# Kernel tuning notes

Hardware: AMD Instinct MI355X
Metric: run time of the kernel (lower is better)

Reference implementation:

```python
import jax, jax.numpy as jnp
import numpy as np

SIZE = 4096       # reservoir width
STEPS = 512       # num_steps
BETA = 1.0        # leak factor (LSMNeuron default beta=1.0)
THRESHOLD = 10.0  # LSMNeuron threshold=10

# Heaviside spike with atan surrogate gradient (snntorch default surrogate)
@jax.custom_vjp
def heaviside(x):
    return (x > 0).astype(x.dtype)

def _h_fwd(x):
    return (x > 0).astype(x.dtype), x

def _h_bwd(x, g):
    # snntorch ATan surrogate with alpha=2: d/dx = 1 / (1 + (pi*x)^2)
    return (g / (1.0 + (jnp.pi * x) ** 2),)

heaviside.defvjp(_h_fwd, _h_bwd)


def setup_inputs() -> dict:
    key = jax.random.key(0)
    kx, kw = jax.random.split(key)
    x = jax.random.normal(kx, (STEPS, SIZE), dtype=jnp.float32)
    # fc1 weight: Linear(2*size, size), no bias. Input half | recurrent half.
    W = jax.random.normal(kw, (SIZE, 2 * SIZE), dtype=jnp.float32) / np.sqrt(2 * SIZE)
    return {"x": x, "W": W}


def reference(x, W):
    # Split weight: Wx acts on the external input, Ws on recurrent spikes.
    Wx = W[:, :SIZE]   # [size, size]
    Ws = W[:, SIZE:]   # [size, size]
    # Precompute the input-driven current for all steps as one big GEMM.
    cur_x = jnp.einsum('ts,os->to', x, Wx)  # [steps, size]

    def step(carry, cur_xt):
        spk, mem = carry
        cur = cur_xt + Ws @ spk            # fc1(concat(x[t], spk))
        mem = BETA * mem + cur             # leaky integrate
        spk = heaviside(mem - THRESHOLD)   # fire
        mem = mem - spk * THRESHOLD        # subtract reset
        return (spk, mem), (spk, mem)

    init = (jnp.zeros((SIZE,), jnp.float32), jnp.zeros((SIZE,), jnp.float32))
    _, (spk_rec, mem_rec) = jax.lax.scan(step, init, cur_x)
    # original detaches spk_rec
    return jax.lax.stop_gradient(spk_rec), mem_rec
```

## Files before the change

### kernel.cpp

```cpp
#include <hip/hip_runtime.h>

#define N_SIZE 4096
#define N_STEPS 512
#define WROW 8192
#define THRESH 10.0f

__global__ __launch_bounds__(256) void k_transpose(const float* __restrict__ W,
                                                   float* __restrict__ WsT) {
    __shared__ float tile[32][33];
    const int bs = blockIdx.x * 32;
    const int bo = blockIdx.y * 32;
    const int tx = threadIdx.x;
    const int ty = threadIdx.y;
#pragma unroll
    for (int j = 0; j < 4; ++j) {
        const int o = bo + ty + j * 8;
        tile[ty + j * 8][tx] = W[(size_t)o * WROW + N_SIZE + bs + tx];
    }
    __syncthreads();
#pragma unroll
    for (int j = 0; j < 4; ++j) {
        const int s = bs + ty + j * 8;
        WsT[(size_t)s * N_SIZE + bo + tx] = tile[tx][ty + j * 8];
    }
}

#define BM 64
#define BN 128
#define BK 16

__global__ __launch_bounds__(256) void k_gemm(const float* __restrict__ x,
                                              const float* __restrict__ W,
                                              float* __restrict__ C) {
    __shared__ float As[BK][BM + 4];
    __shared__ float Bs[BK][BN + 4];
    const int tid = threadIdx.x;
    const int bm = blockIdx.y * BM;
    const int bn = blockIdx.x * BN;
    const int m0 = (tid >> 4) << 2;
    const int n0 = (tid & 15) << 3;
    const int lr = tid >> 2;
    const int lc = (tid & 3) << 2;

    float acc[4][8];
#pragma unroll
    for (int i = 0; i < 4; ++i)
#pragma unroll
        for (int j = 0; j < 8; ++j) acc[i][j] = 0.f;

    for (int kb = 0; kb < N_SIZE; kb += BK) {
        const float4 a  = *(const float4*)&x[(size_t)(bm + lr) * N_SIZE + kb + lc];
        const float4 b0 = *(const float4*)&W[(size_t)(bn + lr) * WROW + kb + lc];
        const float4 b1 = *(const float4*)&W[(size_t)(bn + 64 + lr) * WROW + kb + lc];
        __syncthreads();
        As[lc + 0][lr] = a.x;  As[lc + 1][lr] = a.y;
        As[lc + 2][lr] = a.z;  As[lc + 3][lr] = a.w;
        Bs[lc + 0][lr] = b0.x; Bs[lc + 1][lr] = b0.y;
        Bs[lc + 2][lr] = b0.z; Bs[lc + 3][lr] = b0.w;
        Bs[lc + 0][64 + lr] = b1.x; Bs[lc + 1][64 + lr] = b1.y;
        Bs[lc + 2][64 + lr] = b1.z; Bs[lc + 3][64 + lr] = b1.w;
        __syncthreads();
#pragma unroll
        for (int k = 0; k < BK; ++k) {
            const float4 av  = *(const float4*)&As[k][m0];
            const float4 bv0 = *(const float4*)&Bs[k][n0];
            const float4 bv1 = *(const float4*)&Bs[k][n0 + 4];
            const float am[4]  = {av.x, av.y, av.z, av.w};
            const float bnv[8] = {bv0.x, bv0.y, bv0.z, bv0.w,
                                  bv1.x, bv1.y, bv1.z, bv1.w};
#pragma unroll
            for (int i = 0; i < 4; ++i)
#pragma unroll
                for (int j = 0; j < 8; ++j)
                    acc[i][j] = fmaf(am[i], bnv[j], acc[i][j]);
        }
    }
#pragma unroll
    for (int i = 0; i < 4; ++i) {
        float* cp = &C[(size_t)(bm + m0 + i) * N_SIZE + bn + n0];
        const float4 o0 = {acc[i][0], acc[i][1], acc[i][2], acc[i][3]};
        const float4 o1 = {acc[i][4], acc[i][5], acc[i][6], acc[i][7]};
        *(float4*)&cp[0] = o0;
        *(float4*)&cp[4] = o1;
    }
}

template <int USE_WST>
__global__ __launch_bounds__(1024) void k_scan(const float* __restrict__ WsT,
                                               const float* __restrict__ W,
                                               float* __restrict__ spk_out,
                                               float* __restrict__ mem_out) {
    __shared__ int lists[2][N_SIZE];
    __shared__ int wcnt[16];
    const int tid  = threadIdx.x;
    const int wave = tid >> 6;
    const int lane = tid & 63;
    const int base = tid << 2;

    float4 mem = {0.f, 0.f, 0.f, 0.f};
    int cnt = 0;
    int cur = 0;

    for (int t = 0; t < N_STEPS; ++t) {
        float* mrow = &mem_out[(size_t)t * N_SIZE + base];
        float4 c = *(const float4*)mrow;

        const int* lst = lists[cur];
        int i = 0;
        for (; i + 2 <= cnt; i += 2) {
            const int s0 = lst[i];
            const int s1 = lst[i + 1];
            float4 w0, w1;
            if (USE_WST) {
                w0 = *(const float4*)&WsT[(size_t)s0 * N_SIZE + base];
                w1 = *(const float4*)&WsT[(size_t)s1 * N_SIZE + base];
            } else {
                w0.x = W[(size_t)(base + 0) * WROW + N_SIZE + s0];
                w0.y = W[(size_t)(base + 1) * WROW + N_SIZE + s0];
                w0.z = W[(size_t)(base + 2) * WROW + N_SIZE + s0];
                w0.w = W[(size_t)(base + 3) * WROW + N_SIZE + s0];
                w1.x = W[(size_t)(base + 0) * WROW + N_SIZE + s1];
                w1.y = W[(size_t)(base + 1) * WROW + N_SIZE + s1];
                w1.z = W[(size_t)(base + 2) * WROW + N_SIZE + s1];
                w1.w = W[(size_t)(base + 3) * WROW + N_SIZE + s1];
            }
            c.x += w0.x + w1.x;
            c.y += w0.y + w1.y;
            c.z += w0.z + w1.z;
            c.w += w0.w + w1.w;
        }
        if (i < cnt) {
            const int s0 = lst[i];
            float4 w0;
            if (USE_WST) {
                w0 = *(const float4*)&WsT[(size_t)s0 * N_SIZE + base];
            } else {
                w0.x = W[(size_t)(base + 0) * WROW + N_SIZE + s0];
                w0.y = W[(size_t)(base + 1) * WROW + N_SIZE + s0];
                w0.z = W[(size_t)(base + 2) * WROW + N_SIZE + s0];
                w0.w = W[(size_t)(base + 3) * WROW + N_SIZE + s0];
            }
            c.x += w0.x; c.y += w0.y; c.z += w0.z; c.w += w0.w;
        }

        mem.x += c.x; mem.y += c.y; mem.z += c.z; mem.w += c.w;

        const bool s0 = mem.x > THRESH;
        const bool s1 = mem.y > THRESH;
        const bool s2 = mem.z > THRESH;
        const bool s3 = mem.w > THRESH;
        if (s0) mem.x -= THRESH;
        if (s1) mem.y -= THRESH;
        if (s2) mem.z -= THRESH;
        if (s3) mem.w -= THRESH;

        const float4 spkv = {s0 ? 1.f : 0.f, s1 ? 1.f : 0.f,
                             s2 ? 1.f : 0.f, s3 ? 1.f : 0.f};
        *(float4*)&spk_out[(size_t)t * N_SIZE + base] = spkv;
        *(float4*)mrow = mem;

        const unsigned long long b0 = __ballot(s0);
        const unsigned long long b1 = __ballot(s1);
        const unsigned long long b2 = __ballot(s2);
        const unsigned long long b3 = __ballot(s3);
        const unsigned long long below =
            (lane == 0) ? 0ULL : (~0ULL >> (64 - lane));
        const int pre = __popcll(b0 & below) + __popcll(b1 & below) +
                        __popcll(b2 & below) + __popcll(b3 & below);
        if (lane == 0)
            wcnt[wave] = __popcll(b0) + __popcll(b1) + __popcll(b2) + __popcll(b3);
        __syncthreads();

        int woff = 0, total = 0;
#pragma unroll
        for (int wv = 0; wv < 16; ++wv) {
            const int cw = wcnt[wv];
            woff += (wv < wave) ? cw : 0;
            total += cw;
        }
        int* nxt = lists[cur ^ 1];
        int off = woff + pre;
        if (s0) nxt[off++] = base;
        if (s1) nxt[off++] = base + 1;
        if (s2) nxt[off++] = base + 2;
        if (s3) nxt[off++] = base + 3;
        __syncthreads();

        cnt = total;
        cur ^= 1;
    }
}

extern "C" void kernel_launch(void* const* d_in, const int* in_sizes, int n_in,
                              void* d_out, int out_size, void* d_ws, size_t ws_size,
                              hipStream_t stream) {
    const float* x = (const float*)d_in[0];
    const float* W = (const float*)d_in[1];
    float* spk_out = (float*)d_out;
    float* mem_out = spk_out + (size_t)N_STEPS * N_SIZE;
    float* WsT = (float*)d_ws;
    const bool use_wst = ws_size >= (size_t)N_SIZE * N_SIZE * sizeof(float);

    k_gemm<<<dim3(N_SIZE / BN, N_STEPS / BM), 256, 0, stream>>>(x, W, mem_out);

    if (use_wst) {
        k_transpose<<<dim3(N_SIZE / 32, N_SIZE / 32), dim3(32, 8), 0, stream>>>(W, WsT);
        k_scan<1><<<1, 1024, 0, stream>>>(WsT, W, spk_out, mem_out);
    } else {
        k_scan<0><<<1, 1024, 0, stream>>>(WsT, W, spk_out, mem_out);
    }
}
```

Measured before the change: 1.499 ms.

## Split-K GEMM with register prefetch, 8-wide scan threads, single spike list

The input GEMM now uses 128-thread blocks with 8x8 register tiles, register prefetch of the next K tile, and a split-K over two halves. The second half writes into the spike output buffer and a separate reduce kernel adds it back. The scan kernel drops to 512 threads, each handling 8 neurons, and unrolls the spike-list gather by 4 using masked FMAs. It also prefetches the next step's input current and replaces the double-buffered list with a single list. The aim is more GEMM parallelism and reuse, plus fewer waves and more memory-level parallelism in the serial scan, at the cost of an extra reduce pass and the extra FMA work from padding the gather.

```diff
diff --git a/kernel.cpp b/kernel.cpp
--- a/kernel.cpp
+++ b/kernel.cpp
@@ -13,181 +13,242 @@
     const int tx = threadIdx.x;
     const int ty = threadIdx.y;
 #pragma unroll
-    for (int j = 0; j < 4; ++j) {
-        const int o = bo + ty + j * 8;
-        tile[ty + j * 8][tx] = W[(size_t)o * WROW + N_SIZE + bs + tx];
-    }
+    for (int j = 0; j < 4; ++j)
+        tile[ty + j * 8][tx] = W[(size_t)(bo + ty + j * 8) * WROW + N_SIZE + bs + tx];
     __syncthreads();
 #pragma unroll
-    for (int j = 0; j < 4; ++j) {
-        const int s = bs + ty + j * 8;
-        WsT[(size_t)s * N_SIZE + bo + tx] = tile[tx][ty + j * 8];
-    }
+    for (int j = 0; j < 4; ++j)
+        WsT[(size_t)(bs + ty + j * 8) * N_SIZE + bo + tx] = tile[tx][ty + j * 8];
 }
 
 #define BM 64
 #define BN 128
 #define BK 16
-
-__global__ __launch_bounds__(256) void k_gemm(const float* __restrict__ x,
+#define KHALF (N_SIZE / 2)
+#define ALD 68
+#define BLD 132
+
+#define F4E(v, j) ((j) == 0 ? (v).x : (j) == 1 ? (v).y : (j) == 2 ? (v).z : (v).w)
+
+__global__ __launch_bounds__(128) void k_gemm(const float* __restrict__ x,
                                               const float* __restrict__ W,
-                                              float* __restrict__ C) {
-    __shared__ float As[BK][BM + 4];
-    __shared__ float Bs[BK][BN + 4];
+                                              float* __restrict__ dst0,
+                                              float* __restrict__ dst1) {
+    __shared__ float As[BK][ALD];
+    __shared__ float Bs[BK][BLD];
     const int tid = threadIdx.x;
     const int bm = blockIdx.y * BM;
     const int bn = blockIdx.x * BN;
-    const int m0 = (tid >> 4) << 2;
-    const int n0 = (tid & 15) << 3;
-    const int lr = tid >> 2;
-    const int lc = (tid & 3) << 2;
-
-    float acc[4][8];
-#pragma unroll
-    for (int i = 0; i < 4; ++i)
+    const int kb0 = blockIdx.z * KHALF;
+    float* dst = blockIdx.z ? dst1 : dst0;
+
+    const int m0 = (tid >> 4) << 3;
+    const int n0 = (tid & 15) << 2;
+
+    const int ar = tid >> 2;
+    const int ac = (tid & 3) << 2;
+    const float* Ap = &x[(size_t)(bm + ar) * N_SIZE + kb0 + ac];
+    const float* Bp = &W[(size_t)(bn + ar) * WROW + kb0 + ac];
+
+    float4 pa0 = *(const float4*)&Ap[0];
+    float4 pa1 = *(const float4*)&Ap[(size_t)32 * N_SIZE];
+    float4 pb0 = *(const float4*)&Bp[0];
+    float4 pb1 = *(const float4*)&Bp[(size_t)32 * WROW];
+    float4 pb2 = *(const float4*)&Bp[(size_t)64 * WROW];
+    float4 pb3 = *(const float4*)&Bp[(size_t)96 * WROW];
+
+    float acc[8][8];
+#pragma unroll
+    for (int i = 0; i < 8; ++i)
 #pragma unroll
         for (int j = 0; j < 8; ++j) acc[i][j] = 0.f;
 
-    for (int kb = 0; kb < N_SIZE; kb += BK) {
-        const float4 a  = *(const float4*)&x[(size_t)(bm + lr) * N_SIZE + kb + lc];
-        const float4 b0 = *(const float4*)&W[(size_t)(bn + lr) * WROW + kb + lc];
-        const float4 b1 = *(const float4*)&W[(size_t)(bn + 64 + lr) * WROW + kb + lc];
-        __syncthreads();
-        As[lc + 0][lr] = a.x;  As[lc + 1][lr] = a.y;
-        As[lc + 2][lr] = a.z;  As[lc + 3][lr] = a.w;
-        Bs[lc + 0][lr] = b0.x; Bs[lc + 1][lr] = b0.y;
-        Bs[lc + 2][lr] = b0.z; Bs[lc + 3][lr] = b0.w;
-        Bs[lc + 0][64 + lr] = b1.x; Bs[lc + 1][64 + lr] = b1.y;
-        Bs[lc + 2][64 + lr] = b1.z; Bs[lc + 3][64 + lr] = b1.w;
-        __syncthreads();
+    const int nkt = KHALF / BK;
+    for (int kt = 0; kt < nkt; ++kt) {
+        __syncthreads();
+#pragma unroll
+        for (int j = 0; j < 4; ++j) {
+            As[ac + j][ar]      = F4E(pa0, j);
+            As[ac + j][ar + 32] = F4E(pa1, j);
+            Bs[ac + j][ar]      = F4E(pb0, j);
+            Bs[ac + j][ar + 32] = F4E(pb1, j);
+            Bs[ac + j][ar + 64] = F4E(pb2, j);
+            Bs[ac + j][ar + 96] = F4E(pb3, j);
+        }
+        __syncthreads();
+        if (kt + 1 < nkt) {
+            const float* Ap2 = Ap + (size_t)(kt + 1) * BK;
+            const float* Bp2 = Bp + (size_t)(kt + 1) * BK;
+            pa0 = *(const float4*)&Ap2[0];
+            pa1 = *(const float4*)&Ap2[(size_t)32 * N_SIZE];
+            pb0 = *(const float4*)&Bp2[0];
+            pb1 = *(const float4*)&Bp2[(size_t)32 * WROW];
+            pb2 = *(const float4*)&Bp2[(size_t)64 * WROW];
+            pb3 = *(const float4*)&Bp2[(size_t)96 * WROW];
+        }
 #pragma unroll
         for (int k = 0; k < BK; ++k) {
-            const float4 av  = *(const float4*)&As[k][m0];
-            const float4 bv0 = *(const float4*)&Bs[k][n0];
-            const float4 bv1 = *(const float4*)&Bs[k][n0 + 4];
-            const float am[4]  = {av.x, av.y, av.z, av.w};
-            const float bnv[8] = {bv0.x, bv0.y, bv0.z, bv0.w,
-                                  bv1.x, bv1.y, bv1.z, bv1.w};
-#pragma unroll
-            for (int i = 0; i < 4; ++i)
+            const float4 a0 = *(const float4*)&As[k][m0];
+            const float4 a1 = *(const float4*)&As[k][m0 + 4];
+            const float4 b0 = *(const float4*)&Bs[k][n0];
+            const float4 b1 = *(const float4*)&Bs[k][n0 + 64];
+            const float av[8] = {a0.x, a0.y, a0.z, a0.w, a1.x, a1.y, a1.z, a1.w};
+            const float bv[8] = {b0.x, b0.y, b0.z, b0.w, b1.x, b1.y, b1.z, b1.w};
+#pragma unroll
+            for (int i = 0; i < 8; ++i)
 #pragma unroll
                 for (int j = 0; j < 8; ++j)
-                    acc[i][j] = fmaf(am[i], bnv[j], acc[i][j]);
+                    acc[i][j] = fmaf(av[i], bv[j], acc[i][j]);
         }
     }
 #pragma unroll
-    for (int i = 0; i < 4; ++i) {
-        float* cp = &C[(size_t)(bm + m0 + i) * N_SIZE + bn + n0];
+    for (int i = 0; i < 8; ++i) {
+        float* cp = &dst[(size_t)(bm + m0 + i) * N_SIZE + bn];
         const float4 o0 = {acc[i][0], acc[i][1], acc[i][2], acc[i][3]};
         const float4 o1 = {acc[i][4], acc[i][5], acc[i][6], acc[i][7]};
-        *(float4*)&cp[0] = o0;
-        *(float4*)&cp[4] = o1;
+        *(float4*)&cp[n0] = o0;
+        *(float4*)&cp[n0 + 64] = o1;
     }
 }
 
+__global__ __launch_bounds__(256) void k_reduce(float* __restrict__ acc,
+                                                const float* __restrict__ part) {
+    const size_t i = ((size_t)blockIdx.x * 256 + threadIdx.x) * 4;
+    const float4 a = *(const float4*)&acc[i];
+    const float4 b = *(const float4*)&part[i];
+    const float4 r = {a.x + b.x, a.y + b.y, a.z + b.z, a.w + b.w};
+    *(float4*)&acc[i] = r;
+}
+
 template <int USE_WST>
-__global__ __launch_bounds__(1024) void k_scan(const float* __restrict__ WsT,
-                                               const float* __restrict__ W,
-                                               float* __restrict__ spk_out,
-                                               float* __restrict__ mem_out) {
-    __shared__ int lists[2][N_SIZE];
-    __shared__ int wcnt[16];
-    const int tid  = threadIdx.x;
+__global__ __launch_bounds__(512) void k_scan(const float* __restrict__ WsT,
+                                              const float* __restrict__ W,
+                                              float* __restrict__ spk_out,
+                                              float* __restrict__ mem_out) {
+    __shared__ int lst[N_SIZE];
+    __shared__ int wcnt[8];
+    const int tid = threadIdx.x;
     const int wave = tid >> 6;
     const int lane = tid & 63;
-    const int base = tid << 2;
-
-    float4 mem = {0.f, 0.f, 0.f, 0.f};
+    const int base = tid << 3;
+    const unsigned long long below = (lane == 0) ? 0ULL : (~0ULL >> (64 - lane));
+
+    float4 m0 = {0.f, 0.f, 0.f, 0.f}, m1 = {0.f, 0.f, 0.f, 0.f};
     int cnt = 0;
-    int cur = 0;
+
+    float4 cn0 = *(const float4*)&mem_out[base];
+    float4 cn1 = *(const float4*)&mem_out[base + 4];
 
     for (int t = 0; t < N_STEPS; ++t) {
+        float4 c0 = cn0, c1 = cn1;
+        const int tn = (t + 1 < N_STEPS) ? (t + 1) : t;
+        const float* nr = &mem_out[(size_t)tn * N_SIZE + base];
+        cn0 = *(const float4*)&nr[0];
+        cn1 = *(const float4*)&nr[4];
+
+        for (int i = 0; i < cnt; i += 4) {
+            const int s0 = lst[i];
+            const bool v1 = (i + 1 < cnt), v2 = (i + 2 < cnt), v3 = (i + 3 < cnt);
+            const int s1 = v1 ? lst[i + 1] : s0;
+            const int s2 = v2 ? lst[i + 2] : s0;
+            const int s3 = v3 ? lst[i + 3] : s0;
+            const float f1 = v1 ? 1.f : 0.f;
+            const float f2 = v2 ? 1.f : 0.f;
+            const float f3 = v3 ? 1.f : 0.f;
+            float4 w0a, w0b, w1a, w1b, w2a, w2b, w3a, w3b;
+            if (USE_WST) {
+                const float* p0 = &WsT[(size_t)s0 * N_SIZE + base];
+                const float* p1 = &WsT[(size_t)s1 * N_SIZE + base];
+                const float* p2 = &WsT[(size_t)s2 * N_SIZE + base];
+                const float* p3 = &WsT[(size_t)s3 * N_SIZE + base];
+                w0a = *(const float4*)&p0[0]; w0b = *(const float4*)&p0[4];
+                w1a = *(const float4*)&p1[0]; w1b = *(const float4*)&p1[4];
+                w2a = *(const float4*)&p2[0]; w2b = *(const float4*)&p2[4];
+                w3a = *(const float4*)&p3[0]; w3b = *(const float4*)&p3[4];
+            } else {
+#pragma unroll
+                for (int j = 0; j < 4; ++j) {
+                    F4E(w0a, j) = W[(size_t)(base + j) * WROW + N_SIZE + s0];
+                    F4E(w0b, j) = W[(size_t)(base + 4 + j) * WROW + N_SIZE + s0];
+                    F4E(w1a, j) = W[(size_t)(base + j) * WROW + N_SIZE + s1];
+                    F4E(w1b, j) = W[(size_t)(base + 4 + j) * WROW + N_SIZE + s1];
+                    F4E(w2a, j) = W[(size_t)(base + j) * WROW + N_SIZE + s2];
+                    F4E(w2b, j) = W[(size_t)(base + 4 + j) * WROW + N_SIZE + s2];
+                    F4E(w3a, j) = W[(size_t)(base + j) * WROW + N_SIZE + s3];
+                    F4E(w3b, j) = W[(size_t)(base + 4 + j) * WROW + N_SIZE + s3];
+                }
+            }
+            c0.x += w0a.x; c0.y += w0a.y; c0.z += w0a.z; c0.w += w0a.w;
+            c1.x += w0b.x; c1.y += w0b.y; c1.z += w0b.z; c1.w += w0b.w;
+            c0.x = fmaf(f1, w1a.x, c0.x); c0.y = fmaf(f1, w1a.y, c0.y);
+            c0.z = fmaf(f1, w1a.z, c0.z); c0.w = fmaf(f1, w1a.w, c0.w);
+            c1.x = fmaf(f1, w1b.x, c1.x); c1.y = fmaf(f1, w1b.y, c1.y);
+            c1.z = fmaf(f1, w1b.z, c1.z); c1.w = fmaf(f1, w1b.w, c1.w);
+            c0.x = fmaf(f2, w2a.x, c0.x); c0.y = fmaf(f2, w2a.y, c0.y);
+            c0.z = fmaf(f2, w2a.z, c0.z); c0.w = fmaf(f2, w2a.w, c0.w);
+            c1.x = fmaf(f2, w2b.x, c1.x); c1.y = fmaf(f2, w2b.y, c1.y);
+            c1.z = fmaf(f2, w2b.z, c1.z); c1.w = fmaf(f2, w2b.w, c1.w);
+            c0.x = fmaf(f3, w3a.x, c0.x); c0.y = fmaf(f3, w3a.y, c0.y);
+            c0.z = fmaf(f3, w3a.z, c0.z); c0.w = fmaf(f3, w3a.w, c0.w);
+            c1.x = fmaf(f3, w3b.x, c1.x); c1.y = fmaf(f3, w3b.y, c1.y);
+            c1.z = fmaf(f3, w3b.z, c1.z); c1.w = fmaf(f3, w3b.w, c1.w);
+        }
+
+        m0.x += c0.x; m0.y += c0.y; m0.z += c0.z; m0.w += c0.w;
+        m1.x += c1.x; m1.y += c1.y; m1.z += c1.z; m1.w += c1.w;
+
+        const bool s0b = m0.x > THRESH, s1b = m0.y > THRESH;
+        const bool s2b = m0.z > THRESH, s3b = m0.w > THRESH;
+        const bool s4b = m1.x > THRESH, s5b = m1.y > THRESH;
+        const bool s6b = m1.z > THRESH, s7b = m1.w > THRESH;
+        m0.x -= s0b ? THRESH : 0.f;  m0.y -= s1b ? THRESH : 0.f;
+        m0.z -= s2b ? THRESH : 0.f;  m0.w -= s3b ? THRESH : 0.f;
+        m1.x -= s4b ? THRESH : 0.f;  m1.y -= s5b ? THRESH : 0.f;
+        m1.z -= s6b ? THRESH : 0.f;  m1.w -= s7b ? THRESH : 0.f;
+
+        const float4 sp0 = {s0b ? 1.f : 0.f, s1b ? 1.f : 0.f,
+                            s2b ? 1.f : 0.f, s3b ? 1.f : 0.f};
+        const float4 sp1 = {s4b ? 1.f : 0.f, s5b ? 1.f : 0.f,
+                            s6b ? 1.f : 0.f, s7b ? 1.f : 0.f};
+        float* srow = &spk_out[(size_t)t * N_SIZE + base];
         float* mrow = &mem_out[(size_t)t * N_SIZE + base];
-        float4 c = *(const float4*)mrow;
-
-        const int* lst = lists[cur];
-        int i = 0;
-        for (; i + 2 <= cnt; i += 2) {
-            const int s0 = lst[i];
-            const int s1 = lst[i + 1];
-            float4 w0, w1;
-            if (USE_WST) {
-                w0 = *(const float4*)&WsT[(size_t)s0 * N_SIZE + base];
-                w1 = *(const float4*)&WsT[(size_t)s1 * N_SIZE + base];
-            } else {
-                w0.x = W[(size_t)(base + 0) * WROW + N_SIZE + s0];
-                w0.y = W[(size_t)(base + 1) * WROW + N_SIZE + s0];
-                w0.z = W[(size_t)(base + 2) * WROW + N_SIZE + s0];
-                w0.w = W[(size_t)(base + 3) * WROW + N_SIZE + s0];
-                w1.x = W[(size_t)(base + 0) * WROW + N_SIZE + s1];
-                w1.y = W[(size_t)(base + 1) * WROW + N_SIZE + s1];
-                w1.z = W[(size_t)(base + 2) * WROW + N_SIZE + s1];
-                w1.w = W[(size_t)(base + 3) * WROW + N_SIZE + s1];
-            }
-            c.x += w0.x + w1.x;
-            c.y += w0.y + w1.y;
-            c.z += w0.z + w1.z;
-            c.w += w0.w + w1.w;
-        }
-        if (i < cnt) {
-            const int s0 = lst[i];
-            float4 w0;
-            if (USE_WST) {
-                w0 = *(const float4*)&WsT[(size_t)s0 * N_SIZE + base];
-            } else {
-                w0.x = W[(size_t)(base + 0) * WROW + N_SIZE + s0];
-                w0.y = W[(size_t)(base + 1) * WROW + N_SIZE + s0];
-                w0.z = W[(size_t)(base + 2) * WROW + N_SIZE + s0];
-                w0.w = W[(size_t)(base + 3) * WROW + N_SIZE + s0];
-            }
-            c.x += w0.x; c.y += w0.y; c.z += w0.z; c.w += w0.w;
-        }
-
-        mem.x += c.x; mem.y += c.y; mem.z += c.z; mem.w += c.w;
-
-        const bool s0 = mem.x > THRESH;
-        const bool s1 = mem.y > THRESH;
-        const bool s2 = mem.z > THRESH;
-        const bool s3 = mem.w > THRESH;
-        if (s0) mem.x -= THRESH;
-        if (s1) mem.y -= THRESH;
-        if (s2) mem.z -= THRESH;
-        if (s3) mem.w -= THRESH;
-
-        const float4 spkv = {s0 ? 1.f : 0.f, s1 ? 1.f : 0.f,
-                             s2 ? 1.f : 0.f, s3 ? 1.f : 0.f};
-        *(float4*)&spk_out[(size_t)t * N_SIZE + base] = spkv;
-        *(float4*)mrow = mem;
-
-        const unsigned long long b0 = __ballot(s0);
-        const unsigned long long b1 = __ballot(s1);
-        const unsigned long long b2 = __ballot(s2);
-        const unsigned long long b3 = __ballot(s3);
-        const unsigned long long below =
-            (lane == 0) ? 0ULL : (~0ULL >> (64 - lane));
-        const int pre = __popcll(b0 & below) + __popcll(b1 & below) +
-                        __popcll(b2 & below) + __popcll(b3 & below);
+        *(float4*)&srow[0] = sp0;
+        *(float4*)&srow[4] = sp1;
+        *(float4*)&mrow[0] = m0;
+        *(float4*)&mrow[4] = m1;
+
+        const unsigned long long B0 = __ballot(s0b), B1 = __ballot(s1b);
+        const unsigned long long B2 = __ballot(s2b), B3 = __ballot(s3b);
+        const unsigned long long B4 = __ballot(s4b), B5 = __ballot(s5b);
+        const unsigned long long B6 = __ballot(s6b), B7 = __ballot(s7b);
+        const int pre = __popcll(B0 & below) + __popcll(B1 & below) +
+                        __popcll(B2 & below) + __popcll(B3 & below) +
+                        __popcll(B4 & below) + __popcll(B5 & below) +
+                        __popcll(B6 & below) + __popcll(B7 & below);
         if (lane == 0)
-            wcnt[wave] = __popcll(b0) + __popcll(b1) + __popcll(b2) + __popcll(b3);
+            wcnt[wave] = __popcll(B0) + __popcll(B1) + __popcll(B2) + __popcll(B3) +
+                         __popcll(B4) + __popcll(B5) + __popcll(B6) + __popcll(B7);
         __syncthreads();
 
         int woff = 0, total = 0;
 #pragma unroll
-        for (int wv = 0; wv < 16; ++wv) {
-            const int cw = wcnt[wv];
-            woff += (wv < wave) ? cw : 0;
+        for (int w = 0; w < 8; ++w) {
+            const int cw = wcnt[w];
+            if (w < wave) woff += cw;
             total += cw;
         }
-        int* nxt = lists[cur ^ 1];
         int off = woff + pre;
-        if (s0) nxt[off++] = base;
-        if (s1) nxt[off++] = base + 1;
-        if (s2) nxt[off++] = base + 2;
-        if (s3) nxt[off++] = base + 3;
+        if (s0b) lst[off++] = base + 0;
+        if (s1b) lst[off++] = base + 1;
+        if (s2b) lst[off++] = base + 2;
+        if (s3b) lst[off++] = base + 3;
+        if (s4b) lst[off++] = base + 4;
+        if (s5b) lst[off++] = base + 5;
+        if (s6b) lst[off++] = base + 6;
+        if (s7b) lst[off++] = base + 7;
         __syncthreads();
 
         cnt = total;
-        cur ^= 1;
     }
 }
 
@@ -201,12 +262,14 @@
     float* WsT = (float*)d_ws;
     const bool use_wst = ws_size >= (size_t)N_SIZE * N_SIZE * sizeof(float);
 
-    k_gemm<<<dim3(N_SIZE / BN, N_STEPS / BM), 256, 0, stream>>>(x, W, mem_out);
-
-    if (use_wst) {
+    if (use_wst)
         k_transpose<<<dim3(N_SIZE / 32, N_SIZE / 32), dim3(32, 8), 0, stream>>>(W, WsT);
-        k_scan<1><<<1, 1024, 0, stream>>>(WsT, W, spk_out, mem_out);
-    } else {
-        k_scan<0><<<1, 1024, 0, stream>>>(WsT, W, spk_out, mem_out);
-    }
-}
+
+    k_gemm<<<dim3(N_SIZE / BN, N_STEPS / BM, 2), 128, 0, stream>>>(x, W, mem_out, spk_out);
+    k_reduce<<<(N_STEPS * N_SIZE) / (256 * 4), 256, 0, stream>>>(mem_out, spk_out);
+
+    if (use_wst)
+        k_scan<1><<<1, 512, 0, stream>>>(WsT, W, spk_out, mem_out);
+    else
+        k_scan<0><<<1, 512, 0, stream>>>(WsT, W, spk_out, mem_out);
+}
```

New measurement: 1.499 ms. Within noise of the previous version (-0.0%).
